# Kernel tuning notes

Measured on AMD Instinct MI355X. Metric: run time of the kernel, lower is better.

The kernel has to match this reference:

```python
import jax, jax.numpy as jnp
import numpy as np

B, S, D, H = 2, 2048, 1024, 16
HD = D // H  # 64


def setup_inputs() -> dict:
    key = jax.random.key(0)
    k1, k2, k3, k4, k5, k6 = jax.random.split(key, 6)
    x = jax.random.normal(k1, (B, S, D), dtype=jnp.float32)
    # binary mask source (1.0 = masked-out position), multiplied by -1e9 inside
    mask = (jax.random.uniform(k2, (B, S, S), dtype=jnp.float32) < 0.1).astype(jnp.float32)
    lim = 1.0 / np.sqrt(D)
    Wqkv = jax.random.uniform(k3, (D, 3 * D), dtype=jnp.float32, minval=-lim, maxval=lim)
    bqkv = jax.random.uniform(k4, (3 * D,), dtype=jnp.float32, minval=-lim, maxval=lim)
    Wo = jax.random.uniform(k5, (D, D), dtype=jnp.float32, minval=-lim, maxval=lim)
    bo = jax.random.uniform(k6, (D,), dtype=jnp.float32, minval=-lim, maxval=lim)
    return {"x": x, "mask": mask, "Wqkv": Wqkv, "bqkv": bqkv, "Wo": Wo, "bo": bo}


def reference(x, mask, Wqkv, bqkv, Wo, bo):
    b, s, d = x.shape
    qkv = x @ Wqkv + bqkv                              # [B,S,3D]
    qkv = qkv.reshape(b, s, 3, H, HD).transpose(2, 0, 3, 1, 4)  # [3,B,H,S,HD]
    q, k, v = qkv[0], qkv[1], qkv[2]
    scale = 1.0 / jnp.sqrt(jnp.float32(HD))
    scores = jnp.einsum('bhqd,bhkd->bhqk', q, k) * scale
    scores = scores + mask[:, None, :, :] * (-1e9)     # broadcast over heads
    attn = jax.nn.softmax(scores, axis=-1)             # [B,H,S,S]
    values = jnp.einsum('bhqk,bhkd->bhqd', attn, v)    # [B,H,S,HD]
    # faithful to source: permute(1,0,2,3) then reshape(B,S,H*HD)
    values = values.transpose(1, 0, 2, 3).reshape(b, s, H * HD)
    return values @ Wo + bo
```

## Files before the change

kernel.cpp:

```cpp
#include <hip/hip_runtime.h>
#include <stdint.h>

#define BB 2
#define SS 2048
#define DD 1024
#define HH 16
#define HD 64
#define BH 32
#define BS 4096

typedef short bf16x8 __attribute__((ext_vector_type(8)));
typedef float f32x4 __attribute__((ext_vector_type(4)));

static __device__ __forceinline__ unsigned short f2bf(float f) {
    union { float f; unsigned int u; } x;
    x.f = f;
    unsigned int u = x.u;
    unsigned int r = u + 0x7FFFu + ((u >> 16) & 1u);
    return (unsigned short)(r >> 16);
}

static __device__ __forceinline__ void gld16(unsigned short* lds, const unsigned short* g) {
    __builtin_amdgcn_global_load_lds(
        (const __attribute__((address_space(1))) unsigned int*)g,
        (__attribute__((address_space(3))) unsigned int*)lds,
        16, 0, 0);
}

__global__ __launch_bounds__(256) void prep(
    const float* __restrict__ x, unsigned short* __restrict__ xb,
    const float* __restrict__ Wqkv, unsigned short* __restrict__ WqkvT,
    const float* __restrict__ Wo, unsigned short* __restrict__ WoT,
    const float* __restrict__ mask, unsigned int* __restrict__ mbitsT) {
    __shared__ float tile[32][33];
    int bid = blockIdx.x;
    int tid = threadIdx.x;
    if (bid < 4096) {
        int i = (bid * 256 + tid) * 4;
        float4 v = *(const float4*)(x + i);
        ushort4 o;
        o.x = f2bf(v.x); o.y = f2bf(v.y); o.z = f2bf(v.z); o.w = f2bf(v.w);
        *(ushort4*)(xb + i) = o;
    } else if (bid < 8192) {
        const float* W;
        unsigned short* WT;
        int N, t;
        if (bid < 7168) { W = Wqkv; WT = WqkvT; N = 3072; t = bid - 4096; }
        else            { W = Wo;   WT = WoT;   N = 1024; t = bid - 7168; }
        const int K = 1024;
        int nx = N >> 5;
        int n0 = (t % nx) * 32, k0 = (t / nx) * 32;
        int tx = tid & 31, ty = tid >> 5;
#pragma unroll
        for (int i = 0; i < 4; i++)
            tile[ty + i * 8][tx] = W[(size_t)(k0 + ty + i * 8) * N + n0 + tx];
        __syncthreads();
#pragma unroll
        for (int i = 0; i < 4; i++)
            WT[(size_t)(n0 + ty + i * 8) * K + k0 + tx] = f2bf(tile[tx][ty + i * 8]);
    } else {
        int w = tid >> 6, lane = tid & 63;
        int row = (bid - 8192) * 4 + w;
        int b = row >> 11, sq = row & 2047;
        const float* mrow = mask + ((size_t)b * 2048 + sq) * 2048 + lane * 32;
        unsigned int wbits = 0;
#pragma unroll
        for (int c = 0; c < 8; c++) {
            float4 v = *(const float4*)(mrow + c * 4);
            wbits |= (v.x != 0.0f ? 1u : 0u) << (c * 4);
            wbits |= (v.y != 0.0f ? 2u : 0u) << (c * 4);
            wbits |= (v.z != 0.0f ? 4u : 0u) << (c * 4);
            wbits |= (v.w != 0.0f ? 8u : 0u) << (c * 4);
        }
        mbitsT[((size_t)b * 64 + lane) * 2048 + sq] = wbits;
    }
}

__global__ __launch_bounds__(256) void qkv_gemm(
    const unsigned short* __restrict__ xb,
    const unsigned short* __restrict__ WqkvT,
    const float* __restrict__ bqkv,
    unsigned short* __restrict__ q_ws,
    unsigned short* __restrict__ k_ws,
    unsigned short* __restrict__ vB) {
    __shared__ unsigned short ldsA[4096], ldsB[4096];
    int gxr = blockIdx.x;
    int tid = threadIdx.x;
    int xcd = gxr & 7, lidx = gxr >> 3;
    int m0 = (xcd * 4 + (lidx & 3)) * 128;
    int n0 = (lidx >> 2) * 128;
    int w = tid >> 6, lane = tid & 63, quad = lane >> 4, l15 = lane & 15;

    int r = tid >> 2, p = tid & 3;
    int c = (p - (r >> 1)) & 3;
    const unsigned short* gA0 = xb + (size_t)(m0 + r) * 1024 + c * 8;
    const unsigned short* gA1 = gA0 + (size_t)64 * 1024;
    const unsigned short* gB0 = WqkvT + (size_t)(n0 + r) * 1024 + c * 8;
    const unsigned short* gB1 = gB0 + (size_t)64 * 1024;
    unsigned short* lA0 = ldsA + w * 512;
    unsigned short* lA1 = ldsA + 2048 + w * 512;
    unsigned short* lB0 = ldsB + w * 512;
    unsigned short* lB1 = ldsB + 2048 + w * 512;

    int wm = w >> 1, wn = w & 1;
    int posq = ((quad + (l15 >> 1)) & 3) * 8;
    int aoff = (wm * 64 + l15) * 32 + posq;
    int boff = (wn * 64 + l15) * 32 + posq;

    f32x4 acc[4][4] = {};
    for (int k0 = 0; k0 < 1024; k0 += 32) {
        __syncthreads();
        gld16(lA0, gA0 + k0);
        gld16(lA1, gA1 + k0);
        gld16(lB0, gB0 + k0);
        gld16(lB1, gB1 + k0);
        __syncthreads();
        bf16x8 af[4], bfr[4];
#pragma unroll
        for (int i = 0; i < 4; i++) {
            af[i]  = *(const bf16x8*)(ldsA + aoff + i * 512);
            bfr[i] = *(const bf16x8*)(ldsB + boff + i * 512);
        }
#pragma unroll
        for (int i = 0; i < 4; i++)
#pragma unroll
            for (int j = 0; j < 4; j++)
                acc[i][j] = __builtin_amdgcn_mfma_f32_16x16x32_bf16(af[i], bfr[j], acc[i][j], 0, 0, 0);
    }

    int t = n0 >> 10;
    int ncol0 = n0 + wn * 64;
    int hh = (ncol0 >> 6) & 15;
    int Rb = m0 + wm * 64 + quad * 4;

    if (t == 2) {
        int rowbase = m0 + wm * 64;
        int b = rowbase >> 11;
        int kt = (rowbase >> 6) & 31;
        int bh = b * 16 + hh;
#pragma unroll
        for (int j = 0; j < 4; j++) {
            int hd = j * 16 + l15;
            float bias = bqkv[ncol0 + hd];
#pragma unroll
            for (int i = 0; i < 4; i++) {
                unsigned short* dst = vB +
                    (((((size_t)bh * 32 + kt) * 2 + (i >> 1)) * 4 + quad) * 64 + hd) * 8 + (i & 1) * 4;
                ushort4 pk;
                pk.x = f2bf(acc[i][j][0] + bias);
                pk.y = f2bf(acc[i][j][1] + bias);
                pk.z = f2bf(acc[i][j][2] + bias);
                pk.w = f2bf(acc[i][j][3] + bias);
                *(ushort4*)dst = pk;
            }
        }
    } else {
        unsigned short* dst = (t == 0) ? q_ws : k_ws;
#pragma unroll
        for (int j = 0; j < 4; j++) {
            int hd = j * 16 + l15;
            float bias = bqkv[ncol0 + hd];
#pragma unroll
            for (int i = 0; i < 4; i++) {
                int row = Rb + i * 16;
                int b = row >> 11, s = row & 2047;
                int bh = b * 16 + hh;
#pragma unroll
                for (int rr = 0; rr < 4; rr++)
                    dst[((size_t)(bh * 2048 + s + rr)) * 64 + hd] = f2bf(acc[i][j][rr] + bias);
            }
        }
    }
}

__global__ __launch_bounds__(256) void out_gemm(
    const unsigned short* __restrict__ Amat,
    const unsigned short* __restrict__ WoT,
    const float* __restrict__ bo,
    float* __restrict__ out) {
    __shared__ unsigned short ldsA[4096], ldsB[2048];
    int gxr = blockIdx.x;
    int xcd = gxr & 7, lidx = gxr >> 3;
    int m0 = (xcd * 4 + (lidx & 3)) * 128;
    int n0 = (lidx >> 2) * 64;
    int tid = threadIdx.x;
    int w = tid >> 6, lane = tid & 63, quad = lane >> 4, l15 = lane & 15;

    int r = tid >> 2, p = tid & 3;
    int c = (p - (r >> 1)) & 3;
    const unsigned short* gA0 = Amat + (size_t)(m0 + r) * 1024 + c * 8;
    const unsigned short* gA1 = gA0 + (size_t)64 * 1024;
    const unsigned short* gB0 = WoT + (size_t)(n0 + r) * 1024 + c * 8;
    unsigned short* lA0 = ldsA + w * 512;
    unsigned short* lA1 = ldsA + 2048 + w * 512;
    unsigned short* lB0 = ldsB + w * 512;

    int wm = w >> 1, wn = w & 1;
    int posq = ((quad + (l15 >> 1)) & 3) * 8;
    int aoff = (wm * 64 + l15) * 32 + posq;
    int boff = (wn * 32 + l15) * 32 + posq;

    f32x4 acc[4][2] = {};
    for (int k0 = 0; k0 < 1024; k0 += 32) {
        __syncthreads();
        gld16(lA0, gA0 + k0);
        gld16(lA1, gA1 + k0);
        gld16(lB0, gB0 + k0);
        __syncthreads();
        bf16x8 af[4], bfr[2];
#pragma unroll
        for (int i = 0; i < 4; i++) af[i] = *(const bf16x8*)(ldsA + aoff + i * 512);
#pragma unroll
        for (int j = 0; j < 2; j++) bfr[j] = *(const bf16x8*)(ldsB + boff + j * 512);
#pragma unroll
        for (int i = 0; i < 4; i++)
#pragma unroll
            for (int j = 0; j < 2; j++)
                acc[i][j] = __builtin_amdgcn_mfma_f32_16x16x32_bf16(af[i], bfr[j], acc[i][j], 0, 0, 0);
    }
    int ncol0 = n0 + wn * 32;
    int Rb = m0 + wm * 64 + quad * 4;
#pragma unroll
    for (int j = 0; j < 2; j++) {
        int col = ncol0 + j * 16 + l15;
        float bias = bo[col];
#pragma unroll
        for (int i = 0; i < 4; i++) {
            int row = Rb + i * 16;
#pragma unroll
            for (int rr = 0; rr < 4; rr++)
                out[(size_t)(row + rr) * 1024 + col] = acc[i][j][rr] + bias;
        }
    }
}

__global__ __launch_bounds__(256) void attn(
    const unsigned short* __restrict__ q_ws,
    const unsigned short* __restrict__ k_ws,
    const unsigned short* __restrict__ vB,
    const unsigned int* __restrict__ mbitsT,
    unsigned short* __restrict__ o_ws) {
    __shared__ unsigned short ldsK[8192];
    __shared__ unsigned short ldsV[8192];

    int tid = threadIdx.x;
    int w = tid >> 6, lane = tid & 63, quad = lane >> 4, l15 = lane & 15;
    int bxr = blockIdx.x;
    int bx = ((bxr & 7) << 7) | (bxr >> 3);
    int bh = bx >> 5, qt = bx & 31;
    int b = bh >> 4, h = bh & 15;

    int q = qt * 64 + w * 16 + l15;
    const unsigned short* qptr = q_ws + ((size_t)(bh * 2048 + q)) * 64 + quad * 8;
    bf16x8 qf0 = *(const bf16x8*)(qptr);
    bf16x8 qf1 = *(const bf16x8*)(qptr + 32);

    const float c2 = 0.125f * 1.44269504089f;
    const float Cs = c2 * 8388608.0f;
    const float Ds = (127.0f - 16.0f) * 8388608.0f;

    const unsigned int* mb = mbitsT + (size_t)b * 64 * 2048 + q;
    const unsigned short* kbase = k_ws + (size_t)bh * 2048 * 64;
    const unsigned short* vbb = vB + (size_t)bh * 32 * 4096;

    int srow = (lane >> 3);
    int spos = lane & 7;
    unsigned short* dK0 = ldsK + w * 1024 + lane * 8;
    unsigned short* dV0 = ldsV + w * 1024 + lane * 8;
    int r0 = w * 16 + srow;
    int r1 = r0 + 8;
    int g0 = spos ^ (r0 & 7);
    int g1 = spos ^ (r1 & 7);
    const unsigned short* kS0n = kbase + (size_t)r0 * 64 + g0 * 8;
    const unsigned short* kS1n = kbase + (size_t)r1 * 64 + g1 * 8;
    const unsigned short* vSn  = vbb + (size_t)w * 1024 + lane * 8;
    const unsigned int* mbn = mb;

    f32x4 oacc[4] = {};
    f32x4 lacc = {};
    bf16x8 onesA;
#pragma unroll
    for (int j = 0; j < 8; j++) onesA[j] = (short)0x3F80;

    int sw = (l15 & 7);
    int q4 = quad * 4;

    gld16(dK0, kS0n);
    gld16(dK0 + 512, kS1n);
    gld16(dV0, vSn);
    gld16(dV0 + 512, vSn + 512);
    kS0n += 4096; kS1n += 4096; vSn += 4096;
    unsigned int mw0 = mbn[0];
    unsigned int mw1 = mbn[2048];
    mbn += 4096;
    __syncthreads();

    unsigned int nw0, nw1;

#define ATTN_BODY(KT, CO)                                                          \
    {                                                                              \
        nw0 = 0; nw1 = 0;                                                          \
        if ((KT) < 31) {                 \
            gld16(dK0 + ((CO) ^ 4096), kS0n);                                      \
            gld16(dK0 + ((CO) ^ 4096) + 512, kS1n);                                \
            gld16(dV0 + ((CO) ^ 4096), vSn);                                       \
            gld16(dV0 + ((CO) ^ 4096) + 512, vSn + 512);                           \
            kS0n += 4096; kS1n += 4096; vSn += 4096;                               \
            nw0 = mbn[0]; nw1 = mbn[2048]; mbn += 4096;                            \
        }                                                                          \
        f32x4 sacc[4];                                                             \
        __builtin_amdgcn_s_setprio(1);                                             \
        _Pragma("unroll")                                                          \
        for (int nt = 0; nt < 4; nt++) {                                           \
            const unsigned short* kr = ldsK + (CO) + (nt * 16 + l15) * 64;         \
            bf16x8 kf0, kf1;                                                       \
            __builtin_memcpy(&kf0, kr + (quad ^ sw) * 8, 16);                      \
            __builtin_memcpy(&kf1, kr + ((quad + 4) ^ sw) * 8, 16);                \
            f32x4 z = {};                                                          \
            z = __builtin_amdgcn_mfma_f32_16x16x32_bf16(kf0, qf0, z, 0, 0, 0);     \
            z = __builtin_amdgcn_mfma_f32_16x16x32_bf16(kf1, qf1, z, 0, 0, 0);     \
            sacc[nt] = z;                                                          \
        }                                                                          \
        __builtin_amdgcn_s_setprio(0);                                             \
        unsigned int s0 = mw0 >> q4;                                               \
        unsigned int s1 = mw1 >> q4;                                               \
        unsigned int dw[4][2];                                                     \
        _Pragma("unroll")                                                          \
        for (int nt = 0; nt < 4; nt++) {                                           \
            unsigned int sel = (nt & 2) ? s1 : s0;                                 \
            unsigned int u[4];                                                     \
            _Pragma("unroll")                                                      \
            for (int rr = 0; rr < 4; rr++) {                                       \
                float y = __builtin_fmaf(sacc[nt][rr], Cs, Ds);                    \
                if ((sel >> ((nt & 1) * 16 + rr)) & 1u) y = 0.f;                   \
                u[rr] = (unsigned int)(int)y;                                      \
            }                                                                      \
            dw[nt][0] = __builtin_amdgcn_perm(u[1], u[0], 0x07060302u);            \
            dw[nt][1] = __builtin_amdgcn_perm(u[3], u[2], 0x07060302u);            \
        }                                                                          \
        __builtin_amdgcn_s_setprio(1);                                             \
        _Pragma("unroll")                                                          \
        for (int ks2 = 0; ks2 < 2; ks2++) {                                        \
            union { bf16x8 v; unsigned int d[4]; } bfr;                            \
            bfr.d[0] = dw[2 * ks2][0];                                             \
            bfr.d[1] = dw[2 * ks2][1];                                             \
            bfr.d[2] = dw[2 * ks2 + 1][0];                                         \
            bfr.d[3] = dw[2 * ks2 + 1][1];                                         \
            _Pragma("unroll")                                                      \
            for (int nb = 0; nb < 4; nb++) {                                       \
                bf16x8 vf;                                                         \
                __builtin_memcpy(&vf,                                              \
                    ldsV + (CO) + ((ks2 * 4 + quad) * 64 + nb * 16 + l15) * 8, 16);\
                oacc[nb] = __builtin_amdgcn_mfma_f32_16x16x32_bf16(vf, bfr.v,      \
                                                                   oacc[nb], 0, 0, 0); \
            }                                                                      \
            lacc = __builtin_amdgcn_mfma_f32_16x16x32_bf16(onesA, bfr.v, lacc,     \
                                                           0, 0, 0);               \
        }                                                                          \
        __builtin_amdgcn_s_setprio(0);                                             \
        __syncthreads();               \
        mw0 = nw0; mw1 = nw1;                                                      \
    }

    for (int kt = 0; kt < 32; kt += 2) {
        ATTN_BODY(kt, 0);
        ATTN_BODY(kt + 1, 4096);
    }
#undef ATTN_BODY

    float linv = 1.0f / lacc[0];
    unsigned short* base = o_ws + ((size_t)((h * 2 + b) * 2048 + q)) * 64;
#pragma unroll
    for (int nb = 0; nb < 4; nb++) {
        ushort4 pk;
        pk.x = f2bf(oacc[nb][0] * linv);
        pk.y = f2bf(oacc[nb][1] * linv);
        pk.z = f2bf(oacc[nb][2] * linv);
        pk.w = f2bf(oacc[nb][3] * linv);
        *(ushort4*)(base + nb * 16 + quad * 4) = pk;
    }
}


extern "C" void kernel_launch(void* const* d_in, const int* in_sizes, int n_in,
                              void* d_out, int out_size, void* d_ws, size_t ws_size,
                              hipStream_t stream) {
    const float* x    = (const float*)d_in[0];
    const float* mask = (const float*)d_in[1];
    const float* Wqkv = (const float*)d_in[2];
    const float* bqkv = (const float*)d_in[3];
    const float* Wo   = (const float*)d_in[4];
    const float* bo   = (const float*)d_in[5];
    float* out = (float*)d_out;

    char* ws = (char*)d_ws;
    unsigned short* xb    = (unsigned short*)(ws);
    unsigned short* WqkvT = (unsigned short*)(ws + ((size_t)8 << 20));
    unsigned short* WoT   = (unsigned short*)(ws + ((size_t)14 << 20));
    unsigned short* q_ws  = (unsigned short*)(ws + ((size_t)16 << 20));
    unsigned short* k_ws  = (unsigned short*)(ws + ((size_t)24 << 20));
    unsigned short* vB    = (unsigned short*)(ws + ((size_t)32 << 20));
    unsigned short* o_ws  = (unsigned short*)(ws + ((size_t)40 << 20));
    unsigned int*   mbits = (unsigned int*)(ws + ((size_t)48 << 20));

    prep<<<9216, 256, 0, stream>>>(x, xb, Wqkv, WqkvT, Wo, WoT, mask, mbits);
    qkv_gemm<<<768, 256, 0, stream>>>(xb, WqkvT, bqkv, q_ws, k_ws, vB);
    attn<<<1024, 256, 0, stream>>>(q_ws, k_ws, vB, mbits, o_ws);
    out_gemm<<<512, 256, 0, stream>>>(o_ws, WoT, bo, out);
}
```

Baseline: 225.8 us.

## Move mask bit-packing into QKV GEMM and vectorize epilogue stores via swapped MFMA operands

Mask-to-bitmask packing moves out of the prep kernel and into the tail of the QKV GEMM, where each wave handles rows in a grid-stride loop. The aim is to overlap the mask's memory-bound reads with GEMM compute and to shrink the prep launch. For the Q/K and output GEMMs, the MFMA operand order is swapped so each lane holds four consecutive columns, which allows 8-byte bf16 and 16-byte fp32 vectorized stores instead of scattered scalar ones. This adds mask traffic to the GEMM blocks' tails and duplicates the main loop code.

```diff
diff --git a/kernel.cpp b/kernel.cpp
--- a/kernel.cpp
+++ b/kernel.cpp
@@ -30,8 +30,7 @@
 __global__ __launch_bounds__(256) void prep(
     const float* __restrict__ x, unsigned short* __restrict__ xb,
     const float* __restrict__ Wqkv, unsigned short* __restrict__ WqkvT,
-    const float* __restrict__ Wo, unsigned short* __restrict__ WoT,
-    const float* __restrict__ mask, unsigned int* __restrict__ mbitsT) {
+    const float* __restrict__ Wo, unsigned short* __restrict__ WoT) {
     __shared__ float tile[32][33];
     int bid = blockIdx.x;
     int tid = threadIdx.x;
@@ -41,7 +40,7 @@
         ushort4 o;
         o.x = f2bf(v.x); o.y = f2bf(v.y); o.z = f2bf(v.z); o.w = f2bf(v.w);
         *(ushort4*)(xb + i) = o;
-    } else if (bid < 8192) {
+    } else {
         const float* W;
         unsigned short* WT;
         int N, t;
@@ -58,21 +57,6 @@
 #pragma unroll
         for (int i = 0; i < 4; i++)
             WT[(size_t)(n0 + ty + i * 8) * K + k0 + tx] = f2bf(tile[tx][ty + i * 8]);
-    } else {
-        int w = tid >> 6, lane = tid & 63;
-        int row = (bid - 8192) * 4 + w;
-        int b = row >> 11, sq = row & 2047;
-        const float* mrow = mask + ((size_t)b * 2048 + sq) * 2048 + lane * 32;
-        unsigned int wbits = 0;
-#pragma unroll
-        for (int c = 0; c < 8; c++) {
-            float4 v = *(const float4*)(mrow + c * 4);
-            wbits |= (v.x != 0.0f ? 1u : 0u) << (c * 4);
-            wbits |= (v.y != 0.0f ? 2u : 0u) << (c * 4);
-            wbits |= (v.z != 0.0f ? 4u : 0u) << (c * 4);
-            wbits |= (v.w != 0.0f ? 8u : 0u) << (c * 4);
-        }
-        mbitsT[((size_t)b * 64 + lane) * 2048 + sq] = wbits;
     }
 }
 
@@ -80,6 +64,8 @@
     const unsigned short* __restrict__ xb,
     const unsigned short* __restrict__ WqkvT,
     const float* __restrict__ bqkv,
+    const float* __restrict__ mask,
+    unsigned int* __restrict__ mbitsT,
     unsigned short* __restrict__ q_ws,
     unsigned short* __restrict__ k_ws,
     unsigned short* __restrict__ vB) {
@@ -90,6 +76,7 @@
     int m0 = (xcd * 4 + (lidx & 3)) * 128;
     int n0 = (lidx >> 2) * 128;
     int w = tid >> 6, lane = tid & 63, quad = lane >> 4, l15 = lane & 15;
+    int q4 = quad * 4;
 
     int r = tid >> 2, p = tid & 3;
     int c = (p - (r >> 1)) & 3;
@@ -107,31 +94,52 @@
     int aoff = (wm * 64 + l15) * 32 + posq;
     int boff = (wn * 64 + l15) * 32 + posq;
 
+    int t = n0 >> 10;
     f32x4 acc[4][4] = {};
-    for (int k0 = 0; k0 < 1024; k0 += 32) {
-        __syncthreads();
-        gld16(lA0, gA0 + k0);
-        gld16(lA1, gA1 + k0);
-        gld16(lB0, gB0 + k0);
-        gld16(lB1, gB1 + k0);
-        __syncthreads();
-        bf16x8 af[4], bfr[4];
-#pragma unroll
-        for (int i = 0; i < 4; i++) {
-            af[i]  = *(const bf16x8*)(ldsA + aoff + i * 512);
-            bfr[i] = *(const bf16x8*)(ldsB + boff + i * 512);
-        }
-#pragma unroll
-        for (int i = 0; i < 4; i++)
-#pragma unroll
-            for (int j = 0; j < 4; j++)
-                acc[i][j] = __builtin_amdgcn_mfma_f32_16x16x32_bf16(af[i], bfr[j], acc[i][j], 0, 0, 0);
-    }
-
-    int t = n0 >> 10;
+    if (t == 2) {
+        for (int k0 = 0; k0 < 1024; k0 += 32) {
+            __syncthreads();
+            gld16(lA0, gA0 + k0);
+            gld16(lA1, gA1 + k0);
+            gld16(lB0, gB0 + k0);
+            gld16(lB1, gB1 + k0);
+            __syncthreads();
+            bf16x8 af[4], bfr[4];
+#pragma unroll
+            for (int i = 0; i < 4; i++) {
+                af[i]  = *(const bf16x8*)(ldsA + aoff + i * 512);
+                bfr[i] = *(const bf16x8*)(ldsB + boff + i * 512);
+            }
+#pragma unroll
+            for (int i = 0; i < 4; i++)
+#pragma unroll
+                for (int j = 0; j < 4; j++)
+                    acc[i][j] = __builtin_amdgcn_mfma_f32_16x16x32_bf16(af[i], bfr[j], acc[i][j], 0, 0, 0);
+        }
+    } else {
+        for (int k0 = 0; k0 < 1024; k0 += 32) {
+            __syncthreads();
+            gld16(lA0, gA0 + k0);
+            gld16(lA1, gA1 + k0);
+            gld16(lB0, gB0 + k0);
+            gld16(lB1, gB1 + k0);
+            __syncthreads();
+            bf16x8 af[4], bfr[4];
+#pragma unroll
+            for (int i = 0; i < 4; i++) {
+                af[i]  = *(const bf16x8*)(ldsA + aoff + i * 512);
+                bfr[i] = *(const bf16x8*)(ldsB + boff + i * 512);
+            }
+#pragma unroll
+            for (int i = 0; i < 4; i++)
+#pragma unroll
+                for (int j = 0; j < 4; j++)
+                    acc[i][j] = __builtin_amdgcn_mfma_f32_16x16x32_bf16(bfr[j], af[i], acc[i][j], 0, 0, 0);
+        }
+    }
+
     int ncol0 = n0 + wn * 64;
     int hh = (ncol0 >> 6) & 15;
-    int Rb = m0 + wm * 64 + quad * 4;
 
     if (t == 2) {
         int rowbase = m0 + wm * 64;
@@ -156,19 +164,40 @@
         }
     } else {
         unsigned short* dst = (t == 0) ? q_ws : k_ws;
+        int sBase = m0 + wm * 64;
 #pragma unroll
         for (int j = 0; j < 4; j++) {
-            int hd = j * 16 + l15;
-            float bias = bqkv[ncol0 + hd];
+            float4 b4 = *(const float4*)(bqkv + ncol0 + j * 16 + q4);
 #pragma unroll
             for (int i = 0; i < 4; i++) {
-                int row = Rb + i * 16;
+                int row = sBase + i * 16 + l15;
                 int b = row >> 11, s = row & 2047;
                 int bh = b * 16 + hh;
-#pragma unroll
-                for (int rr = 0; rr < 4; rr++)
-                    dst[((size_t)(bh * 2048 + s + rr)) * 64 + hd] = f2bf(acc[i][j][rr] + bias);
+                ushort4 pk;
+                pk.x = f2bf(acc[i][j][0] + b4.x);
+                pk.y = f2bf(acc[i][j][1] + b4.y);
+                pk.z = f2bf(acc[i][j][2] + b4.z);
+                pk.w = f2bf(acc[i][j][3] + b4.w);
+                *(ushort4*)(dst + ((size_t)(bh * 2048 + s)) * 64 + j * 16 + q4) = pk;
             }
+        }
+    }
+
+    {
+        int wid = gxr * 4 + w;
+        for (int row = wid; row < 4096; row += 3072) {
+            const float* mrow = mask + (size_t)row * 2048 + lane * 32;
+            unsigned int wbits = 0;
+#pragma unroll
+            for (int cc = 0; cc < 8; cc++) {
+                float4 v = *(const float4*)(mrow + cc * 4);
+                wbits |= (v.x != 0.0f ? 1u : 0u) << (cc * 4);
+                wbits |= (v.y != 0.0f ? 2u : 0u) << (cc * 4);
+                wbits |= (v.z != 0.0f ? 4u : 0u) << (cc * 4);
+                wbits |= (v.w != 0.0f ? 8u : 0u) << (cc * 4);
+            }
+            int b = row >> 11, sq = row & 2047;
+            mbitsT[((size_t)b * 64 + lane) * 2048 + sq] = wbits;
         }
     }
 }
@@ -185,6 +214,7 @@
     int n0 = (lidx >> 2) * 64;
     int tid = threadIdx.x;
     int w = tid >> 6, lane = tid & 63, quad = lane >> 4, l15 = lane & 15;
+    int q4 = quad * 4;
 
     int r = tid >> 2, p = tid & 3;
     int c = (p - (r >> 1)) & 3;
@@ -216,20 +246,22 @@
         for (int i = 0; i < 4; i++)
 #pragma unroll
             for (int j = 0; j < 2; j++)
-                acc[i][j] = __builtin_amdgcn_mfma_f32_16x16x32_bf16(af[i], bfr[j], acc[i][j], 0, 0, 0);
+                acc[i][j] = __builtin_amdgcn_mfma_f32_16x16x32_bf16(bfr[j], af[i], acc[i][j], 0, 0, 0);
     }
     int ncol0 = n0 + wn * 32;
-    int Rb = m0 + wm * 64 + quad * 4;
+    int rBase = m0 + wm * 64;
 #pragma unroll
     for (int j = 0; j < 2; j++) {
-        int col = ncol0 + j * 16 + l15;
-        float bias = bo[col];
+        float4 b4 = *(const float4*)(bo + ncol0 + j * 16 + q4);
 #pragma unroll
         for (int i = 0; i < 4; i++) {
-            int row = Rb + i * 16;
-#pragma unroll
-            for (int rr = 0; rr < 4; rr++)
-                out[(size_t)(row + rr) * 1024 + col] = acc[i][j][rr] + bias;
+            int row = rBase + i * 16 + l15;
+            float4 o4;
+            o4.x = acc[i][j][0] + b4.x;
+            o4.y = acc[i][j][1] + b4.y;
+            o4.z = acc[i][j][2] + b4.z;
+            o4.w = acc[i][j][3] + b4.w;
+            *(float4*)(out + (size_t)row * 1024 + ncol0 + j * 16 + q4) = o4;
         }
     }
 }
@@ -403,8 +435,8 @@
     unsigned short* o_ws  = (unsigned short*)(ws + ((size_t)40 << 20));
     unsigned int*   mbits = (unsigned int*)(ws + ((size_t)48 << 20));
 
-    prep<<<9216, 256, 0, stream>>>(x, xb, Wqkv, WqkvT, Wo, WoT, mask, mbits);
-    qkv_gemm<<<768, 256, 0, stream>>>(xb, WqkvT, bqkv, q_ws, k_ws, vB);
+    prep<<<8192, 256, 0, stream>>>(x, xb, Wqkv, WqkvT, Wo, WoT);
+    qkv_gemm<<<768, 256, 0, stream>>>(xb, WqkvT, bqkv, mask, mbits, q_ws, k_ws, vB);
     attn<<<1024, 256, 0, stream>>>(q_ws, k_ws, vB, mbits, o_ws);
     out_gemm<<<512, 256, 0, stream>>>(o_ws, WoT, bo, out);
 }
```

Result: faster. 221.0 us, median of 2 (-2.1%).
